# Kernel optimization log

Measured on AMD Instinct MI355X. Metric: run time of the kernel, lower is better.

Reference implementation:

```python
import jax, jax.numpy as jnp
import numpy as np


def setup_inputs() -> dict:
    key = jax.random.key(0)
    B, N = 32, 262144
    z = jax.random.uniform(key, (B, N, 3), dtype=jnp.float32)
    return {"z": z}


def reference(z):
    # order == 'xyz': lexicographic sort of the N points by (x, y, z),
    # x most significant. jnp.lexsort treats the LAST key as primary,
    # so pass (z_key, y_key, x_key). Sorts along axis=-1 (points),
    # batched over B for free.
    keys = (z[:, :, 2], z[:, :, 1], z[:, :, 0])  # each [B, N]
    idx_pa = jnp.lexsort(keys, axis=-1)          # [B, N] permutation: sorted -> original
    # Original computes torch.sort(gather(arange, idx_pa))[1], which is the
    # inverse permutation of idx_pa; argsort of a permutation inverts it.
    idx_re = jnp.argsort(idx_pa, axis=-1)        # [B, N] original -> sorted position
    return idx_pa, idx_re
```

## Files before the change

### kernel.cpp

```cpp
#include <hip/hip_runtime.h>
#include <stdint.h>

typedef unsigned int u32;
typedef unsigned long long u64;
typedef unsigned char u8;

#define BROWS 32
#define NPTS  262144
#define LOG_NPTS 18
#define CB 256
#define RCAP 1280
#define ROWSTRIDE_FIX (CB * RCAP)
#define CCAP 1536
#define FB2 1024

#define MCH 4096
#define MWG 512
#define TCH 8192
#define TWG 1024

__device__ __forceinline__ u32 g18_of(float z0) {
    int b = (int)(z0 * 262144.0f);
    return (u32)(b < 0 ? 0 : (b > 262143 ? 262143 : b));
}

__global__ __launch_bounds__(256) void hist_kernel(const float* __restrict__ z,
                                                   u32* __restrict__ counts) {
    __shared__ u32 h[CB];
    for (int i = threadIdx.x; i < CB; i += 256) h[i] = 0;
    __syncthreads();
    int r = blockIdx.x >> 6;
    int c = blockIdx.x & 63;
    size_t base = ((size_t)r << LOG_NPTS) + (size_t)c * 4096;
    for (int k = 0; k < 16; ++k) {
        float z0 = z[(base + (size_t)(k * 256 + threadIdx.x)) * 3];
        atomicAdd(&h[g18_of(z0) >> 10], 1u);
    }
    __syncthreads();
    for (int i = threadIdx.x; i < CB; i += 256)
        if (h[i]) atomicAdd(&counts[r * CB + i], h[i]);
}

__global__ __launch_bounds__(256) void scan_dense(const u32* __restrict__ counts,
                                                  u32* __restrict__ offsets,
                                                  u32* __restrict__ gcur) {
    int r = blockIdx.x, t = threadIdx.x;
    __shared__ u32 sc[CB];
    u32 v = counts[r * CB + t];
    sc[t] = v;
    __syncthreads();
    u32 own = v;
    for (int off = 1; off < CB; off <<= 1) {
        u32 a = (t >= off) ? sc[t - off] : 0;
        __syncthreads();
        sc[t] += a;
        __syncthreads();
    }
    u32 ex = sc[t] - own;
    offsets[r * CB + t] = ex;
    gcur[r * CB + t] = ex;
}

__global__ void init_fixed(u32* __restrict__ gcur) {
    int i = blockIdx.x * 256 + threadIdx.x;
    gcur[i] = (u32)(i & 255) * RCAP;
}

__global__ __launch_bounds__(256) void scan_fixed(const u32* __restrict__ gcur,
                                                  u32* __restrict__ offsets,
                                                  u32* __restrict__ counts) {
    int r = blockIdx.x, t = threadIdx.x;
    __shared__ u32 sc[CB];
    u32 cnt = gcur[r * CB + t] - (u32)t * RCAP;
    if (cnt > RCAP) cnt = RCAP;
    counts[r * CB + t] = cnt;
    sc[t] = cnt;
    __syncthreads();
    u32 own = cnt;
    for (int off = 1; off < CB; off <<= 1) {
        u32 a = (t >= off) ? sc[t - off] : 0;
        __syncthreads();
        sc[t] += a;
        __syncthreads();
    }
    offsets[r * CB + t] = sc[t] - own;
}

__global__ __launch_bounds__(MWG) void ms_scatter(const float* __restrict__ z,
                                                  u32* __restrict__ gcur,
                                                  ulonglong2* __restrict__ recKV,
                                                  int fixedMode) {
    __shared__ u32 h[CB], sc[CB], gb[CB];
    __shared__ ulonglong2 rKV[MCH];
    int t = threadIdx.x;
    int r = blockIdx.x >> 6;
    int c = blockIdx.x & 63;
    if (t < CB) h[t] = 0;
    __syncthreads();
    u64 mh[8], ml[8];
    u32 mpk[8];
    size_t zbase = (((size_t)r << LOG_NPTS) + (size_t)c * MCH) * 3;
#pragma unroll
    for (int k = 0; k < 8; ++k) {
        u32 i = (u32)(c * MCH + k * MWG + t);
        const float* p = z + zbase + (size_t)(k * MWG + t) * 3;
        float f0 = p[0], f1 = p[1], f2 = p[2];
        u32 k0 = __float_as_uint(f0), k1 = __float_as_uint(f1), k2 = __float_as_uint(f2);
        mh[k] = ((u64)k0 << 32) | k1;
        ml[k] = ((u64)k2 << 32) | i;
        u32 b = g18_of(f0) >> 10;
        u32 arr = atomicAdd(&h[b], 1u);
        mpk[k] = (b << 16) | arr;
    }
    __syncthreads();
    if (t < CB) sc[t] = h[t];
    __syncthreads();
    for (int off = 1; off < CB; off <<= 1) {
        u32 a = 0;
        if (t < CB && t >= off) a = sc[t - off];
        __syncthreads();
        if (t < CB) sc[t] += a;
        __syncthreads();
    }
    if (t < CB) {
        sc[t] -= h[t];
        gb[t] = atomicAdd(&gcur[r * CB + t], h[t]);
    }
    __syncthreads();
#pragma unroll
    for (int k = 0; k < 8; ++k) {
        u32 b = mpk[k] >> 16, arr = mpk[k] & 0xFFFFu;
        u32 p = sc[b] + arr;
        rKV[p].x = mh[k];
        rKV[p].y = ml[k];
    }
    __syncthreads();
    size_t rowrec = fixedMode ? (size_t)r * ROWSTRIDE_FIX : ((size_t)r << LOG_NPTS);
#pragma unroll
    for (int k = 0; k < 8; ++k) {
        u32 s = (u32)(k * MWG + t);
        ulonglong2 v = rKV[s];
        u32 b = g18_of(__uint_as_float((u32)(v.x >> 32))) >> 10;
        u32 local = s - sc[b];
        u32 dst = gb[b] + local;
        if (!fixedMode || dst < b * (u32)RCAP + (u32)RCAP)
            recKV[rowrec + dst] = v;
    }
}

__global__ __launch_bounds__(256) void fine_sort(const ulonglong2* __restrict__ recKV,
                                                 const u32* __restrict__ offsets,
                                                 const u32* __restrict__ counts,
                                                 int* __restrict__ out_pa,
                                                 int fixedMode) {
    __shared__ ulonglong2 kv2[CCAP];
    __shared__ u32 fh[FB2], fex[FB2], wtot[4];
    int t = threadIdx.x;
    int g = blockIdx.x;
    int r = g >> 8;
    int cbk = g & 255;
    size_t rowrec = fixedMode ? (size_t)r * ROWSTRIDE_FIX : ((size_t)r << LOG_NPTS);
    u32 rdstart = fixedMode ? (u32)cbk * RCAP : offsets[g];
    u32 wrstart = offsets[g];
    u32 count = counts[g];
    u32 cap = fixedMode ? (u32)RCAP : (u32)CCAP;
    if (count > cap) count = cap;
    for (int i = t; i < FB2; i += 256) fh[i] = 0;
    __syncthreads();

    u64 rh[6], rl[6];
    u32 rpk[6];
#pragma unroll
    for (int k = 0; k < 6; ++k) {
        u32 s = (u32)t + (u32)k * 256u;
        rpk[k] = 0xFFFFFFFFu;
        if (s < count) {
            ulonglong2 rec = recKV[rowrec + rdstart + s];
            rh[k] = rec.x; rl[k] = rec.y;
            u32 fb = g18_of(__uint_as_float((u32)(rec.x >> 32))) & (FB2 - 1);
            u32 arr = atomicAdd(&fh[fb], 1u);
            rpk[k] = (fb << 16) | arr;
        }
    }
    __syncthreads();
    {
        u32 v0 = fh[4 * t], v1 = fh[4 * t + 1], v2 = fh[4 * t + 2], v3 = fh[4 * t + 3];
        u32 tsum = v0 + v1 + v2 + v3;
        u32 s = tsum;
        int lane = t & 63, w = t >> 6;
        for (int off = 1; off < 64; off <<= 1) {
            u32 o = __shfl_up(s, off, 64);
            if (lane >= off) s += o;
        }
        if (lane == 63) wtot[w] = s;
        __syncthreads();
        u32 wbase = 0;
        if (w > 0) wbase += wtot[0];
        if (w > 1) wbase += wtot[1];
        if (w > 2) wbase += wtot[2];
        u32 ex = wbase + s - tsum;
        fex[4 * t] = ex;
        fex[4 * t + 1] = ex + v0;
        fex[4 * t + 2] = ex + v0 + v1;
        fex[4 * t + 3] = ex + v0 + v1 + v2;
    }
    __syncthreads();
#pragma unroll
    for (int k = 0; k < 6; ++k) {
        if (rpk[k] != 0xFFFFFFFFu) {
            u32 fb = rpk[k] >> 16, arr = rpk[k] & 0xFFFFu;
            u32 p = fex[fb] + arr;
            kv2[p].x = rh[k];
            kv2[p].y = rl[k];
        }
    }
    __syncthreads();

    size_t orow = (size_t)r << LOG_NPTS;
#pragma unroll
    for (int k = 0; k < 6; ++k) {
        if (rpk[k] == 0xFFFFFFFFu) continue;
        u32 fb = rpk[k] >> 16;
        u32 cnt = fh[fb];
        u32 rank = 0;
        if (cnt > 1) {
            u32 base = fex[fb];
            for (u32 j = 0; j < cnt; ++j) {
                ulonglong2 b2 = kv2[base + j];
                rank += (b2.x < rh[k]) || (b2.x == rh[k] && b2.y < rl[k]);
            }
        }
        u32 pos = fex[fb] + rank;
        out_pa[orow + wrstart + pos] = (int)(u32)(rl[k] & 0x3FFFFu);
    }
}

__global__ __launch_bounds__(TWG) void trans_ms(const int* __restrict__ out_pa,
                                                u32* __restrict__ tcur,
                                                u32* __restrict__ pairs) {
    __shared__ u32 h[CB], sc[CB], gb[CB];
    __shared__ u32 reord[TCH];
    __shared__ u8 rb8[TCH];
    int t = threadIdx.x;
    int r = blockIdx.x >> 5;
    int c = blockIdx.x & 31;
    if (t < CB) h[t] = 0;
    __syncthreads();
    u32 mpk[8], mv[8];
#pragma unroll
    for (int k = 0; k < 8; ++k) {
        u32 p = (u32)(c * TCH + k * TWG + t);
        u32 si = (u32)out_pa[((size_t)r << LOG_NPTS) + p];
        u32 b = si >> 10;
        mv[k] = ((si & 1023u) << 18) | p;
        u32 arr = atomicAdd(&h[b], 1u);
        mpk[k] = (b << 16) | arr;
    }
    __syncthreads();
    if (t < CB) sc[t] = h[t];
    __syncthreads();
    for (int off = 1; off < CB; off <<= 1) {
        u32 a = 0;
        if (t < CB && t >= off) a = sc[t - off];
        __syncthreads();
        if (t < CB) sc[t] += a;
        __syncthreads();
    }
    if (t < CB) {
        sc[t] -= h[t];
        gb[t] = atomicAdd(&tcur[r * CB + t], h[t]);
    }
    __syncthreads();
#pragma unroll
    for (int k = 0; k < 8; ++k) {
        u32 b = mpk[k] >> 16, arr = mpk[k] & 0xFFFFu;
        u32 p = sc[b] + arr;
        reord[p] = mv[k];
        rb8[p] = (u8)b;
    }
    __syncthreads();
#pragma unroll
    for (int k = 0; k < 8; ++k) {
        u32 s = (u32)(k * TWG + t);
        u32 v = reord[s];
        u32 b = rb8[s];
        u32 local = s - sc[b];
        pairs[((size_t)r << LOG_NPTS) + (size_t)b * 1024 + gb[b] + local] = v;
    }
}

__global__ __launch_bounds__(256) void trans_write(const u32* __restrict__ pairs,
                                                   int* __restrict__ out_re) {
    __shared__ u32 buf[1024];
    int g = blockIdx.x;
    int r = g >> 8, b = g & 255;
    size_t base = ((size_t)r << LOG_NPTS) + (size_t)b * 1024;
#pragma unroll
    for (int k = 0; k < 4; ++k) {
        u32 v = pairs[base + (size_t)(k * 256 + threadIdx.x)];
        buf[v >> 18] = v & 0x3FFFFu;
    }
    __syncthreads();
#pragma unroll
    for (int k = 0; k < 4; ++k) {
        int j = k * 256 + threadIdx.x;
        out_re[base + (size_t)j] = (int)buf[j];
    }
}

extern "C" void kernel_launch(void* const* d_in, const int* in_sizes, int n_in,
                              void* d_out, int out_size, void* d_ws, size_t ws_size,
                              hipStream_t stream) {
    const float* z = (const float*)d_in[0];
    int* out_pa = (int*)d_out;
    int* out_re = out_pa + (size_t)BROWS * NPTS;

    char* ws = (char*)d_ws;
    u32* counts  = (u32*)(ws);
    u32* offsets = (u32*)(ws + (64u << 10));
    u32* gcur    = (u32*)(ws + (128u << 10));
    u32* tcur    = (u32*)(ws + (192u << 10));
    ulonglong2* recKV = (ulonglong2*)(ws + (1u << 20));
    u32* pairs   = (u32*)recKV;

    size_t need = (1ull << 20) + (size_t)BROWS * CB * RCAP * sizeof(ulonglong2);
    int fixedMode = (ws_size >= need) ? 1 : 0;

    hipMemsetAsync(tcur, 0, (size_t)BROWS * CB * sizeof(u32), stream);
    if (fixedMode) {
        init_fixed<<<BROWS, 256, 0, stream>>>(gcur);
        ms_scatter<<<BROWS * 64, MWG, 0, stream>>>(z, gcur, recKV, 1);
        scan_fixed<<<BROWS, 256, 0, stream>>>(gcur, offsets, counts);
        fine_sort<<<BROWS * CB, 256, 0, stream>>>(recKV, offsets, counts, out_pa, 1);
    } else {
        hipMemsetAsync(counts, 0, (size_t)BROWS * CB * sizeof(u32), stream);
        hist_kernel<<<BROWS * 64, 256, 0, stream>>>(z, counts);
        scan_dense<<<BROWS, 256, 0, stream>>>(counts, offsets, gcur);
        ms_scatter<<<BROWS * 64, MWG, 0, stream>>>(z, gcur, recKV, 0);
        fine_sort<<<BROWS * CB, 256, 0, stream>>>(recKV, offsets, counts, out_pa, 0);
    }
    trans_ms<<<BROWS * 32, TWG, 0, stream>>>(out_pa, tcur, pairs);
    trans_write<<<BROWS * CB, 256, 0, stream>>>(pairs, out_re);
}
```

Before: 162.6 us.

## Scatter directly to global without LDS reordering; fold tcur zeroing into init

Drops the shared-memory local reorder (block scan plus staging buffer) in the multisplit scatter and transpose kernels. Each element is now written straight to its global slot using its atomic arrival index. Chunk size and workgroup size in ms_scatter are doubled. The tcur memset is folded into init_fixed, removing a launch. This saves LDS traffic, barriers and the block scan, but global writes become less coalesced because elements of the same bucket are no longer contiguous across lanes.

```diff
diff --git a/kernel.cpp b/kernel.cpp
--- a/kernel.cpp
+++ b/kernel.cpp
@@ -14,8 +14,8 @@
 #define CCAP 1536
 #define FB2 1024
 
-#define MCH 4096
-#define MWG 512
+#define MCH 8192
+#define MWG 1024
 #define TCH 8192
 #define TWG 1024
 
@@ -61,9 +61,10 @@
     gcur[r * CB + t] = ex;
 }
 
-__global__ void init_fixed(u32* __restrict__ gcur) {
+__global__ void init_fixed(u32* __restrict__ gcur, u32* __restrict__ tcur) {
     int i = blockIdx.x * 256 + threadIdx.x;
     gcur[i] = (u32)(i & 255) * RCAP;
+    tcur[i] = 0;
 }
 
 __global__ __launch_bounds__(256) void scan_fixed(const u32* __restrict__ gcur,
@@ -90,11 +91,10 @@
                                                   u32* __restrict__ gcur,
                                                   ulonglong2* __restrict__ recKV,
                                                   int fixedMode) {
-    __shared__ u32 h[CB], sc[CB], gb[CB];
-    __shared__ ulonglong2 rKV[MCH];
+    __shared__ u32 h[CB], gb[CB];
     int t = threadIdx.x;
-    int r = blockIdx.x >> 6;
-    int c = blockIdx.x & 63;
+    int r = blockIdx.x >> 5;
+    int c = blockIdx.x & 31;
     if (t < CB) h[t] = 0;
     __syncthreads();
     u64 mh[8], ml[8];
@@ -113,38 +113,18 @@
         mpk[k] = (b << 16) | arr;
     }
     __syncthreads();
-    if (t < CB) sc[t] = h[t];
-    __syncthreads();
-    for (int off = 1; off < CB; off <<= 1) {
-        u32 a = 0;
-        if (t < CB && t >= off) a = sc[t - off];
-        __syncthreads();
-        if (t < CB) sc[t] += a;
-        __syncthreads();
-    }
-    if (t < CB) {
-        sc[t] -= h[t];
+    if (t < CB)
         gb[t] = atomicAdd(&gcur[r * CB + t], h[t]);
-    }
-    __syncthreads();
+    __syncthreads();
+    size_t rowrec = fixedMode ? (size_t)r * ROWSTRIDE_FIX : ((size_t)r << LOG_NPTS);
 #pragma unroll
     for (int k = 0; k < 8; ++k) {
         u32 b = mpk[k] >> 16, arr = mpk[k] & 0xFFFFu;
-        u32 p = sc[b] + arr;
-        rKV[p].x = mh[k];
-        rKV[p].y = ml[k];
-    }
-    __syncthreads();
-    size_t rowrec = fixedMode ? (size_t)r * ROWSTRIDE_FIX : ((size_t)r << LOG_NPTS);
-#pragma unroll
-    for (int k = 0; k < 8; ++k) {
-        u32 s = (u32)(k * MWG + t);
-        ulonglong2 v = rKV[s];
-        u32 b = g18_of(__uint_as_float((u32)(v.x >> 32))) >> 10;
-        u32 local = s - sc[b];
-        u32 dst = gb[b] + local;
-        if (!fixedMode || dst < b * (u32)RCAP + (u32)RCAP)
+        u32 dst = gb[b] + arr;
+        if (!fixedMode || dst < (b + 1u) * (u32)RCAP) {
+            ulonglong2 v; v.x = mh[k]; v.y = ml[k];
             recKV[rowrec + dst] = v;
+        }
     }
 }
 
@@ -238,9 +218,7 @@
 __global__ __launch_bounds__(TWG) void trans_ms(const int* __restrict__ out_pa,
                                                 u32* __restrict__ tcur,
                                                 u32* __restrict__ pairs) {
-    __shared__ u32 h[CB], sc[CB], gb[CB];
-    __shared__ u32 reord[TCH];
-    __shared__ u8 rb8[TCH];
+    __shared__ u32 h[CB], gb[CB];
     int t = threadIdx.x;
     int r = blockIdx.x >> 5;
     int c = blockIdx.x & 31;
@@ -257,35 +235,14 @@
         mpk[k] = (b << 16) | arr;
     }
     __syncthreads();
-    if (t < CB) sc[t] = h[t];
-    __syncthreads();
-    for (int off = 1; off < CB; off <<= 1) {
-        u32 a = 0;
-        if (t < CB && t >= off) a = sc[t - off];
-        __syncthreads();
-        if (t < CB) sc[t] += a;
-        __syncthreads();
-    }
-    if (t < CB) {
-        sc[t] -= h[t];
+    if (t < CB)
         gb[t] = atomicAdd(&tcur[r * CB + t], h[t]);
-    }
-    __syncthreads();
+    __syncthreads();
+    size_t prow = (size_t)r << LOG_NPTS;
 #pragma unroll
     for (int k = 0; k < 8; ++k) {
         u32 b = mpk[k] >> 16, arr = mpk[k] & 0xFFFFu;
-        u32 p = sc[b] + arr;
-        reord[p] = mv[k];
-        rb8[p] = (u8)b;
-    }
-    __syncthreads();
-#pragma unroll
-    for (int k = 0; k < 8; ++k) {
-        u32 s = (u32)(k * TWG + t);
-        u32 v = reord[s];
-        u32 b = rb8[s];
-        u32 local = s - sc[b];
-        pairs[((size_t)r << LOG_NPTS) + (size_t)b * 1024 + gb[b] + local] = v;
+        pairs[prow + (size_t)b * 1024 + gb[b] + arr] = mv[k];
     }
 }
 
@@ -326,17 +283,17 @@
     size_t need = (1ull << 20) + (size_t)BROWS * CB * RCAP * sizeof(ulonglong2);
     int fixedMode = (ws_size >= need) ? 1 : 0;
 
-    hipMemsetAsync(tcur, 0, (size_t)BROWS * CB * sizeof(u32), stream);
     if (fixedMode) {
-        init_fixed<<<BROWS, 256, 0, stream>>>(gcur);
-        ms_scatter<<<BROWS * 64, MWG, 0, stream>>>(z, gcur, recKV, 1);
+        init_fixed<<<BROWS, 256, 0, stream>>>(gcur, tcur);
+        ms_scatter<<<BROWS * 32, MWG, 0, stream>>>(z, gcur, recKV, 1);
         scan_fixed<<<BROWS, 256, 0, stream>>>(gcur, offsets, counts);
         fine_sort<<<BROWS * CB, 256, 0, stream>>>(recKV, offsets, counts, out_pa, 1);
     } else {
         hipMemsetAsync(counts, 0, (size_t)BROWS * CB * sizeof(u32), stream);
+        hipMemsetAsync(tcur, 0, (size_t)BROWS * CB * sizeof(u32), stream);
         hist_kernel<<<BROWS * 64, 256, 0, stream>>>(z, counts);
         scan_dense<<<BROWS, 256, 0, stream>>>(counts, offsets, gcur);
-        ms_scatter<<<BROWS * 64, MWG, 0, stream>>>(z, gcur, recKV, 0);
+        ms_scatter<<<BROWS * 32, MWG, 0, stream>>>(z, gcur, recKV, 0);
         fine_sort<<<BROWS * CB, 256, 0, stream>>>(recKV, offsets, counts, out_pa, 0);
     }
     trans_ms<<<BROWS * 32, TWG, 0, stream>>>(out_pa, tcur, pairs);
```

Measured after the change: 211.1 us. 1.3x slower.
